# Performance work log

Measured on AMD Instinct MI355X. Metric: run time of the kernel, lower is better.

The kernel has to match this reference:

```python
import jax, jax.numpy as jnp
import numpy as np

NR, NA = 2, 1                 # num_raw, num_angle
QDIM = NR + 2 * NA            # 4: [r, x1=cos(th), x2=sin(th)]
DQ = NR + NA                  # 3: [dr, dth]
D = 2 * NR + 3 * NA           # 7: full state dim
HID = 256
EPS = 1e-6


def setup_inputs() -> dict:
    key = jax.random.key(0)
    ks = jax.random.split(key, 4)
    B = 32768
    x = jax.random.normal(ks[0], (B, D), dtype=jnp.float32)
    W0 = jax.random.normal(ks[1], (HID, D), dtype=jnp.float32) / np.sqrt(D)
    b0 = jnp.zeros((HID,), dtype=jnp.float32)
    W1 = jax.random.normal(ks[2], (HID, HID), dtype=jnp.float32) / np.sqrt(HID)
    b1 = jnp.zeros((HID,), dtype=jnp.float32)
    W2 = jax.random.normal(ks[3], (1, HID), dtype=jnp.float32) / np.sqrt(HID)
    b2 = jnp.zeros((1,), dtype=jnp.float32)
    return {"x": x, "W0": W0, "b0": b0, "W1": W1, "b1": b1, "W2": W2, "b2": b2}


def _lnn_forward(x, W0, b0, W1, b1, W2, b2):
    def L_single(xi):  # scalar Lagrangian of one state (D,)
        h = jnp.tanh(W0 @ xi + b0)
        h = jnp.tanh(W1 @ h + b1)
        return (W2 @ h + b2)[0]

    grad_single = jax.grad(L_single)
    gradL = jax.vmap(grad_single)(x)                       # (B, D)

    # Rows of the Hessian corresponding to d/d(dr,dth): (B, DQ, D).
    # Replaces the torch per-row autograd.grad loop with one batched jacfwd.
    def g(xi):
        return grad_single(xi)[QDIM:]                      # dL/d(dr,dth), (DQ,)
    Hrows = jax.vmap(jax.jacfwd(g))(x)                     # (B, DQ, D)

    x1 = x[:, NR:NR + NA]                                  # cos part (B, NA)
    x2 = x[:, NR + NA:QDIM]                                # sin part (B, NA)

    Jr = Hrows[:, :, :NR]                                  # (B, DQ, NR)
    Jx1 = Hrows[:, :, NR:NR + NA]                          # (B, DQ, NA)
    Jx2 = Hrows[:, :, NR + NA:QDIM]                        # (B, DQ, NA)
    Hdq = Hrows[:, :, QDIM:] + EPS * jnp.eye(DQ, dtype=x.dtype)  # (B, DQ, DQ)

    # chain rule back to angle theta: d/dth = -x2 * d/dx1 + x1 * d/dx2
    Jth = -x2[:, None, :] * Jx1 + x1[:, None, :] * Jx2     # (B, DQ, NA)
    Jrth = jnp.concatenate([Jr, Jth], axis=2)              # (B, DQ, DQ)

    dLdr = gradL[:, :NR]
    dLdx1 = gradL[:, NR:NR + NA]
    dLdx2 = gradL[:, NR + NA:QDIM]
    dLdth = -x2 * dLdx1 + x1 * dLdx2
    dLdrdth = jnp.concatenate([dLdr, dLdth], axis=1)       # (B, DQ)

    dq = x[:, QDIM:]                                       # (B, DQ)
    dq_term = jnp.einsum('bij,bj->bi', Jrth, dq)

    rhs = dLdrdth - dq_term                                # control = 0 (no controlNet)
    ddq = jnp.linalg.solve(Hdq, rhs[..., None])[..., 0]    # (B, DQ)

    dr = dq[:, :NR]
    dth = dq[:, NR:]
    dx1 = -x2 * dth
    dx2 = x1 * dth
    return jnp.concatenate([dr, dx1, dx2, ddq], axis=1)    # (B, D)


def reference(x, W0, b0, W1, b1, W2, b2):
    return _lnn_forward(x, W0, b0, W1, b1, W2, b2)
```

## Files before the change

kernel.cpp:

```cpp
#include <hip/hip_runtime.h>
#include <math.h>

#define HID 256
#define EPS_REG 1e-6

typedef __attribute__((ext_vector_type(8))) short short8;
typedef __attribute__((ext_vector_type(4))) short short4v;
typedef __attribute__((ext_vector_type(4))) float v4f;

#define MFMA_BF16(a, b, c) __builtin_amdgcn_mfma_f32_16x16x32_bf16((a), (b), (c), 0, 0, 0)

__device__ __forceinline__ float fast_tanh(float z) {
    const float e = __expf(2.0f * z);
    const float d = e + 1.0f;
    float r = __builtin_amdgcn_rcpf(d);
    r = r * (2.0f - d * r);
    return fmaf(-2.0f, r, 1.0f);
}

__device__ __forceinline__ float rtn_bf16(float v, short* s) {
    unsigned r = (__float_as_uint(v) + 0x8000u) & 0xFFFF0000u;
    *s = (short)(r >> 16);
    return __uint_as_float(r);
}
__device__ __forceinline__ void split3(float v, short* a, short* b, short* c) {
    float f0 = rtn_bf16(v, a);
    float r1 = v - f0;
    float f1 = rtn_bf16(r1, b);
    float r2 = r1 - f1;
    (void)rtn_bf16(r2, c);
}

__global__ void prep_w1_frags(const float* __restrict__ W1, short* __restrict__ ws) {
    const int gid   = blockIdx.x * 128 + threadIdx.x;
    const int lane  = gid & 63;
    const int ks    = (gid >> 6) & 7;
    const int rt    = (gid >> 9) & 15;
    const int which = gid >> 13;
    const int m = lane & 15, q = lane >> 4;

    float v[8];
    if (which == 0) {
        const float* p = W1 + (size_t)(rt*16 + m)*HID + ks*32 + q*8;
        const float4 va = *(const float4*)(p);
        const float4 vb = *(const float4*)(p + 4);
        v[0]=va.x; v[1]=va.y; v[2]=va.z; v[3]=va.w;
        v[4]=vb.x; v[5]=vb.y; v[6]=vb.z; v[7]=vb.w;
    } else {
        const float* p = W1 + (size_t)(ks*32 + q*8)*HID + rt*16 + m;
#pragma unroll
        for (int t = 0; t < 8; ++t) v[t] = p[(size_t)t*HID];
    }
    short8 h8, m8, l8;
#pragma unroll
    for (int t = 0; t < 8; ++t) {
        short sh, sm, sl;
        split3(v[t], &sh, &sm, &sl);
        h8[t] = sh; m8[t] = sm; l8[t] = sl;
    }
    const size_t base = (size_t)which*3*65536 + ((size_t)(rt*8 + ks)*64 + lane)*8;
    *(short8*)(ws + base)          = h8;
    *(short8*)(ws + base + 65536)  = m8;
    *(short8*)(ws + base + 131072) = l8;
}

#define FRAG_NT_STRIDE 13056
#define FRAG_BUF_STRIDE 4352
#define BFRAG_SHORTS 26112
#define M0H_FLOATS 2304
#define PIPE_LDS_BYTES 122880

__device__ __forceinline__ void lnn_phase0(const float* __restrict__ x,
    const float* __restrict__ W0, const float* __restrict__ b0,
    int samp_base, short* __restrict__ Bf, float* __restrict__ M0, int tid)
{
    const int j  = tid & 255;
    const int s0 = (tid >> 8) * 4;
    float w0r[7];
#pragma unroll
    for (int d = 0; d < 7; ++d) w0r[d] = W0[j*7 + d];
    const float bj = b0[j];
    const int kbase = (j >> 3)*136 + (j & 7);
#pragma unroll
    for (int si = 0; si < 4; ++si) {
        const int s = s0 + si;
        const float* xs = x + (size_t)(samp_base + s)*7;
        float z = bj;
#pragma unroll
        for (int d = 0; d < 7; ++d) z = fmaf(w0r[d], xs[d], z);
        const float h  = fast_tanh(z);
        const float sg = 1.0f - h*h;
        M0[j*9 + s] = h;
        const int nt = s >> 2;
        const int cb = (s & 3) * 4;
        float vals[4] = {h, sg*w0r[4], sg*w0r[5], sg*w0r[6]};
#pragma unroll
        for (int comp = 0; comp < 4; ++comp) {
            short sh, sm, sl;
            split3(vals[comp], &sh, &sm, &sl);
            const int a = nt*FRAG_NT_STRIDE + kbase + (cb + comp)*8;
            Bf[a]                     = sh;
            Bf[a + FRAG_BUF_STRIDE]   = sm;
            Bf[a + 2*FRAG_BUF_STRIDE] = sl;
        }
    }
}

__device__ __forceinline__ void lnn_mm(const short8* __restrict__ Ah,
    const short8* __restrict__ Am, const short8* __restrict__ Al,
    const short* __restrict__ Bf, int w, int lane, int boff, v4f acc[2][2])
{
    short8 pah[2][2], pam[2][2], pal[2][2];
#pragma unroll
    for (int rtl = 0; rtl < 2; ++rtl) {
        const size_t fi = ((size_t)((w*2 + rtl)*8))*64 + lane;
        pah[0][rtl] = Ah[fi]; pam[0][rtl] = Am[fi]; pal[0][rtl] = Al[fi];
    }
#pragma unroll
    for (int ks = 0; ks < 8; ++ks) {
        const int cur = ks & 1, nxt = cur ^ 1;
        if (ks < 7) {
#pragma unroll
            for (int rtl = 0; rtl < 2; ++rtl) {
                const size_t fi = ((size_t)((w*2 + rtl)*8 + ks + 1))*64 + lane;
                pah[nxt][rtl] = Ah[fi]; pam[nxt][rtl] = Am[fi]; pal[nxt][rtl] = Al[fi];
            }
        }
        short8 bh[2], bm[2], bl[2];
#pragma unroll
        for (int nt = 0; nt < 2; ++nt) {
            const int a = nt*FRAG_NT_STRIDE + ks*544 + boff;
            bh[nt] = *(const short8*)(&Bf[a]);
            bm[nt] = *(const short8*)(&Bf[a + FRAG_BUF_STRIDE]);
            bl[nt] = *(const short8*)(&Bf[a + 2*FRAG_BUF_STRIDE]);
        }
#pragma unroll
        for (int rtl = 0; rtl < 2; ++rtl) {
            const short8 ah = pah[cur][rtl];
            const short8 am = pam[cur][rtl];
            const short8 al = pal[cur][rtl];
#pragma unroll
            for (int nt = 0; nt < 2; ++nt) {
                acc[rtl][nt] = MFMA_BF16(ah, bl[nt], acc[rtl][nt]);
                acc[rtl][nt] = MFMA_BF16(al, bh[nt], acc[rtl][nt]);
                acc[rtl][nt] = MFMA_BF16(am, bm[nt], acc[rtl][nt]);
                acc[rtl][nt] = MFMA_BF16(am, bh[nt], acc[rtl][nt]);
                acc[rtl][nt] = MFMA_BF16(ah, bm[nt], acc[rtl][nt]);
                acc[rtl][nt] = MFMA_BF16(ah, bh[nt], acc[rtl][nt]);
            }
        }
    }
}

__device__ __forceinline__ void lnn_epi1(v4f acc[2][2], short* __restrict__ Bf,
    const float* __restrict__ b1, const float* __restrict__ W2,
    int w, int lane, int q, int c)
{
    const int myreg = c & 3;
#pragma unroll
    for (int rtl = 0; rtl < 2; ++rtl) {
        const int base = (w*2 + rtl)*16;
        float b1r[4], w2r[4];
#pragma unroll
        for (int r = 0; r < 4; ++r) {
            b1r[r] = b1[base + q*4 + r];
            w2r[r] = W2[base + q*4 + r];
        }
        const int G  = (base >> 3) + (q >> 1);
        const int tq = (q & 1) * 4;
#pragma unroll
        for (int nt = 0; nt < 2; ++nt) {
            short4v ph, pm, pl;
#pragma unroll
            for (int r = 0; r < 4; ++r) {
                const float z0 = __shfl(acc[rtl][nt][r] + b1r[r], lane & ~3, 64);
                const float h1 = fast_tanh(z0);
                const float s1 = 1.0f - h1*h1;
                const float av = acc[rtl][nt][r];
                const float u  = (myreg == 0) ? (w2r[r]*s1)
                                              : (-2.0f*w2r[r]*h1*s1)*av;
                short sh, sm, sl;
                split3(u, &sh, &sm, &sl);
                ph[r] = sh; pm[r] = sm; pl[r] = sl;
            }
            const int a = nt*FRAG_NT_STRIDE + G*136 + c*8 + tq;
            *(short4v*)(&Bf[a])                     = ph;
            *(short4v*)(&Bf[a + FRAG_BUF_STRIDE])   = pm;
            *(short4v*)(&Bf[a + 2*FRAG_BUF_STRIDE]) = pl;
        }
    }
}

__device__ __forceinline__ void lnn_epi2(v4f acc2[2][2], short* __restrict__ Bf,
    const float* __restrict__ M0, const float* __restrict__ W0,
    int w, int lane, int q, int c)
{
    float* U0 = (float*)Bf;
#pragma unroll
    for (int rtl = 0; rtl < 2; ++rtl) {
#pragma unroll
        for (int reg = 0; reg < 4; ++reg) {
            const int j = (w*2 + rtl)*16 + q*4 + reg;
            const float w0sel = W0[j*7 + 3 + (c & 3)];
#pragma unroll
            for (int nt = 0; nt < 2; ++nt) {
                const int s = nt*4 + (c >> 2);
                const float pv = acc2[rtl][nt][reg];
                const float p0 = __shfl(pv, lane & ~3, 64);
                const float h0 = M0[j*9 + s];
                const float sg = 1.0f - h0*h0;
                const float t2 = -2.0f * p0 * h0 * sg;
                const float res = ((c & 3) == 0) ? (p0*sg)
                                                 : fmaf(pv, sg, t2 * w0sel);
                U0[j*36 + s*4 + (c & 3)] = res;
            }
        }
    }
}

__device__ __forceinline__ void lnn_phase3(const float* __restrict__ x,
    const float* __restrict__ W0, short* __restrict__ Bf,
    int samp_base, float* __restrict__ out, int w, int tid)
{
    const float* U0 = (const float*)Bf;
    float* scratch = ((float*)Bf) + 9216 + w * 425;
    const int t = tid & 63;
    float part[25];
#pragma unroll
    for (int qq = 0; qq < 25; ++qq) part[qq] = 0.0f;

#pragma unroll
    for (int m = 0; m < 4; ++m) {
        const int j = t + 64*m;
        const float4 uv = *(const float4*)(&U0[j*36 + w*4]);
        float w0d[7];
#pragma unroll
        for (int d = 0; d < 7; ++d) w0d[d] = W0[j*7 + d];
#pragma unroll
        for (int d = 0; d < 4; ++d) part[d] = fmaf(uv.x, w0d[d], part[d]);
#pragma unroll
        for (int d = 0; d < 7; ++d) {
            part[4  + d] = fmaf(uv.y, w0d[d], part[4  + d]);
            part[11 + d] = fmaf(uv.z, w0d[d], part[11 + d]);
            part[18 + d] = fmaf(uv.w, w0d[d], part[18 + d]);
        }
    }
#pragma unroll
    for (int off = 1; off <= 2; off <<= 1)
#pragma unroll
        for (int qq = 0; qq < 25; ++qq)
            part[qq] += __shfl_xor(part[qq], off, 64);
    {
        const int quad = t >> 2;
        if ((t & 3) == 0) {
#pragma unroll
            for (int e = 0; e < 25; ++e)
                scratch[e*17 + quad] = part[e];
        }
    }
    if (t < 25) {
        float tot = 0.0f;
#pragma unroll
        for (int k = 0; k < 16; ++k) tot += scratch[t*17 + k];
        scratch[t*17 + 16] = tot;
    }

    if (t == 0) {
        double g[25];
#pragma unroll
        for (int e = 0; e < 25; ++e) g[e] = (double)scratch[e*17 + 16];

        const float* xs = x + (size_t)(samp_base + w)*7;
        const double x1 = xs[2], x2 = xs[3];
        const double dq0 = xs[4], dq1 = xs[5], dth = xs[6];

        double M[3][3], rhs[3];
#pragma unroll
        for (int i = 0; i < 3; ++i) {
            const double J0 = g[4 + i*7 + 0];
            const double J1 = g[4 + i*7 + 1];
            const double J2 = -x2*g[4 + i*7 + 2] + x1*g[4 + i*7 + 3];
            const double dL = (i == 0) ? g[0]
                            : (i == 1) ? g[1]
                            : (-x2*g[2] + x1*g[3]);
            M[i][0] = g[4 + i*7 + 4] + (i == 0 ? EPS_REG : 0.0);
            M[i][1] = g[4 + i*7 + 5] + (i == 1 ? EPS_REG : 0.0);
            M[i][2] = g[4 + i*7 + 6] + (i == 2 ? EPS_REG : 0.0);
            rhs[i]  = dL - (J0*dq0 + J1*dq1 + J2*dth);
        }
        const double c00 = M[1][1]*M[2][2] - M[1][2]*M[2][1];
        const double c01 = M[1][2]*M[2][0] - M[1][0]*M[2][2];
        const double c02 = M[1][0]*M[2][1] - M[1][1]*M[2][0];
        const double det = M[0][0]*c00 + M[0][1]*c01 + M[0][2]*c02;
        const double inv = 1.0 / det;
        const double c10 = M[0][2]*M[2][1] - M[0][1]*M[2][2];
        const double c11 = M[0][0]*M[2][2] - M[0][2]*M[2][0];
        const double c12 = M[0][1]*M[2][0] - M[0][0]*M[2][1];
        const double c20 = M[0][1]*M[1][2] - M[0][2]*M[1][1];
        const double c21 = M[0][2]*M[1][0] - M[0][0]*M[1][2];
        const double c22 = M[0][0]*M[1][1] - M[0][1]*M[1][0];
        const double sol0 = (c00*rhs[0] + c10*rhs[1] + c20*rhs[2]) * inv;
        const double sol1 = (c01*rhs[0] + c11*rhs[1] + c21*rhs[2]) * inv;
        const double sol2 = (c02*rhs[0] + c12*rhs[1] + c22*rhs[2]) * inv;

        float* o = out + (size_t)(samp_base + w)*7;
        o[0] = (float)dq0;
        o[1] = (float)dq1;
        o[2] = (float)(-x2*dth);
        o[3] = (float)( x1*dth);
        o[4] = (float)sol0;
        o[5] = (float)sol1;
        o[6] = (float)sol2;
    }
}

__global__ __launch_bounds__(1024, 4)
void lnn_pipe(const float* __restrict__ x,
              const float* __restrict__ W0, const float* __restrict__ b0,
              const float* __restrict__ b1, const float* __restrict__ W2,
              const short* __restrict__ ws,
              float* __restrict__ out)
{
    extern __shared__ __align__(16) short smem[];

    const int tid  = threadIdx.x;
    const int w16  = tid >> 6;
    const int isA  = (w16 < 8) ? 1 : 0;
    const int w    = w16 & 7;
    const int lane = tid & 63;
    const int gtid = w*64 + lane;

    short* Bf = smem + (isA ? 0 : BFRAG_SHORTS);
    float* M0 = (float*)(smem + 2*BFRAG_SHORTS) + (isA ? 0 : M0H_FLOATS);
    const int samp0 = blockIdx.x * 16 + (isA ? 0 : 8);

    const short8* A1h = (const short8*)ws;
    const short8* A1m = A1h + 8192;
    const short8* A1l = A1h + 16384;
    const short8* A2h = A1h + 24576;
    const short8* A2m = A1h + 32768;
    const short8* A2l = A1h + 40960;

    const int q = lane >> 4;
    const int c = lane & 15;
    const int boff = q*136 + c*8;

    if (isA) lnn_phase0(x, W0, b0, samp0, Bf, M0, gtid);
    __syncthreads();

    v4f acc[2][2];
#pragma unroll
    for (int r = 0; r < 2; ++r)
#pragma unroll
        for (int n = 0; n < 2; ++n) acc[r][n] = (v4f){0.f, 0.f, 0.f, 0.f};
    if (isA) lnn_mm(A1h, A1m, A1l, Bf, w, lane, boff, acc);
    else     lnn_phase0(x, W0, b0, samp0, Bf, M0, gtid);
    __syncthreads();

    if (isA) lnn_epi1(acc, Bf, b1, W2, w, lane, q, c);
    else     lnn_mm(A1h, A1m, A1l, Bf, w, lane, boff, acc);
    __syncthreads();

    v4f acc2[2][2];
#pragma unroll
    for (int r = 0; r < 2; ++r)
#pragma unroll
        for (int n = 0; n < 2; ++n) acc2[r][n] = (v4f){0.f, 0.f, 0.f, 0.f};
    if (isA) lnn_mm(A2h, A2m, A2l, Bf, w, lane, boff, acc2);
    else     lnn_epi1(acc, Bf, b1, W2, w, lane, q, c);
    __syncthreads();

    if (isA) lnn_epi2(acc2, Bf, M0, W0, w, lane, q, c);
    else     lnn_mm(A2h, A2m, A2l, Bf, w, lane, boff, acc2);
    __syncthreads();

    if (isA) lnn_phase3(x, W0, Bf, samp0, out, w, gtid);
    else     lnn_epi2(acc2, Bf, M0, W0, w, lane, q, c);
    __syncthreads();

    if (!isA) lnn_phase3(x, W0, Bf, samp0, out, w, gtid);
}

__global__ __launch_bounds__(512, 4)
void lnn_mfma(const float* __restrict__ x,
              const float* __restrict__ W0, const float* __restrict__ b0,
              const float* __restrict__ b1, const float* __restrict__ W2,
              const short* __restrict__ ws,
              float* __restrict__ out)
{
    __shared__ __align__(16) short Bfrag[26112];
    __shared__ float M0h[HID * 9];

    const int tid   = threadIdx.x;
    const int samp0 = blockIdx.x * 8;
    const int lane  = tid & 63;
    const int w     = tid >> 6;

    lnn_phase0(x, W0, b0, samp0, Bfrag, M0h, tid);
    __syncthreads();

    const short8* A1h = (const short8*)ws;
    const short8* A1m = A1h + 8192;
    const short8* A1l = A1h + 16384;
    const short8* A2h = A1h + 24576;
    const short8* A2m = A1h + 32768;
    const short8* A2l = A1h + 40960;

    const int q = lane >> 4;
    const int c = lane & 15;
    const int boff = q*136 + c*8;

    v4f acc[2][2];
#pragma unroll
    for (int r = 0; r < 2; ++r)
#pragma unroll
        for (int n = 0; n < 2; ++n) acc[r][n] = (v4f){0.f, 0.f, 0.f, 0.f};
    lnn_mm(A1h, A1m, A1l, Bfrag, w, lane, boff, acc);
    __syncthreads();

    lnn_epi1(acc, Bfrag, b1, W2, w, lane, q, c);
    __syncthreads();

    v4f acc2[2][2];
#pragma unroll
    for (int r = 0; r < 2; ++r)
#pragma unroll
        for (int n = 0; n < 2; ++n) acc2[r][n] = (v4f){0.f, 0.f, 0.f, 0.f};
    lnn_mm(A2h, A2m, A2l, Bfrag, w, lane, boff, acc2);
    __syncthreads();

    lnn_epi2(acc2, Bfrag, M0h, W0, w, lane, q, c);
    __syncthreads();

    lnn_phase3(x, W0, Bfrag, samp0, out, w, tid);
}

#define TS8 8
#define SCP 36

__global__ void transpose_w1(const float* __restrict__ W1, float* __restrict__ W1T) {
    __shared__ float tile[32][33];
    const int bx = blockIdx.x & 7;
    const int by = blockIdx.x >> 3;
    const int tx = threadIdx.x & 31;
    const int ty = threadIdx.x >> 5;
#pragma unroll
    for (int q = 0; q < 4; ++q)
        tile[ty + q*8][tx] = W1[(by*32 + ty + q*8)*HID + bx*32 + tx];
    __syncthreads();
#pragma unroll
    for (int q = 0; q < 4; ++q)
        W1T[(bx*32 + ty + q*8)*HID + by*32 + tx] = tile[tx][ty + q*8];
}

__global__ __launch_bounds__(256, 2)
void lnn_fused(const float* __restrict__ x,
               const float* __restrict__ W0, const float* __restrict__ b0,
               const float* __restrict__ W1, const float* __restrict__ b1,
               const float* __restrict__ W2,
               const float* __restrict__ W1T, const int useT,
               float* __restrict__ out)
{
    __shared__ float M0[HID * SCP];
    __shared__ float U [HID * SCP];
    const int tid   = threadIdx.x;
    const int samp0 = blockIdx.x * TS8;
    {
        const int j = tid;
        float w0r[7];
#pragma unroll
        for (int d = 0; d < 7; ++d) w0r[d] = W0[j*7 + d];
        const float bj = b0[j];
#pragma unroll
        for (int s = 0; s < TS8; ++s) {
            const float* xs = x + (size_t)(samp0 + s)*7;
            float z = bj;
#pragma unroll
            for (int d = 0; d < 7; ++d) z = fmaf(w0r[d], xs[d], z);
            const float h  = tanhf(z);
            const float sg = 1.0f - h*h;
            float4 v = {h, sg * w0r[4], sg * w0r[5], sg * w0r[6]};
            *(float4*)(&M0[j*SCP + s*4]) = v;
        }
    }
    __syncthreads();
    const int it = tid & 63;
    const int ct = tid >> 6;
    float acc[4][8];
#pragma unroll
    for (int r = 0; r < 4; ++r)
#pragma unroll
        for (int c = 0; c < 8; ++c) acc[r][c] = 0.0f;
    if (useT) {
#pragma unroll 4
        for (int j = 0; j < HID; ++j) {
            const float4 w4 = *(const float4*)(W1T + (size_t)j*HID + it*4);
            const float4 ma = *(const float4*)(&M0[j*SCP + ct*8]);
            const float4 mb = *(const float4*)(&M0[j*SCP + ct*8 + 4]);
            const float w[4] = {w4.x, w4.y, w4.z, w4.w};
            const float m[8] = {ma.x, ma.y, ma.z, ma.w, mb.x, mb.y, mb.z, mb.w};
#pragma unroll
            for (int r = 0; r < 4; ++r)
#pragma unroll
                for (int c = 0; c < 8; ++c)
                    acc[r][c] = fmaf(w[r], m[c], acc[r][c]);
        }
    } else {
#pragma unroll 2
        for (int j = 0; j < HID; ++j) {
            float w[4];
#pragma unroll
            for (int r = 0; r < 4; ++r) w[r] = W1[(size_t)(it*4 + r)*HID + j];
            const float4 ma = *(const float4*)(&M0[j*SCP + ct*8]);
            const float4 mb = *(const float4*)(&M0[j*SCP + ct*8 + 4]);
            const float m[8] = {ma.x, ma.y, ma.z, ma.w, mb.x, mb.y, mb.z, mb.w};
#pragma unroll
            for (int r = 0; r < 4; ++r)
#pragma unroll
                for (int c = 0; c < 8; ++c)
                    acc[r][c] = fmaf(w[r], m[c], acc[r][c]);
        }
    }
    {
#pragma unroll
        for (int r = 0; r < 4; ++r) {
            const int i = it*4 + r;
            const float b1i = b1[i];
            const float w2i = W2[i];
#pragma unroll
            for (int cs = 0; cs < 2; ++cs) {
                const float z1 = acc[r][cs*4+0] + b1i;
                const float h1 = tanhf(z1);
                const float s1 = 1.0f - h1*h1;
                float4 uv;
                uv.x = w2i * s1;
                const float m2 = -2.0f * w2i * h1 * s1;
                uv.y = m2 * acc[r][cs*4+1];
                uv.z = m2 * acc[r][cs*4+2];
                uv.w = m2 * acc[r][cs*4+3];
                *(float4*)(&U[i*SCP + ct*8 + cs*4]) = uv;
            }
        }
    }
    __syncthreads();
    float acc2[4][8];
#pragma unroll
    for (int r = 0; r < 4; ++r)
#pragma unroll
        for (int c = 0; c < 8; ++c) acc2[r][c] = 0.0f;
#pragma unroll 4
    for (int i = 0; i < HID; ++i) {
        const float4 w4 = *(const float4*)(W1 + (size_t)i*HID + it*4);
        const float4 ua = *(const float4*)(&U[i*SCP + ct*8]);
        const float4 ub = *(const float4*)(&U[i*SCP + ct*8 + 4]);
        const float w[4] = {w4.x, w4.y, w4.z, w4.w};
        const float m[8] = {ua.x, ua.y, ua.z, ua.w, ub.x, ub.y, ub.z, ub.w};
#pragma unroll
        for (int r = 0; r < 4; ++r)
#pragma unroll
            for (int c = 0; c < 8; ++c)
                acc2[r][c] = fmaf(w[r], m[c], acc2[r][c]);
    }
    __syncthreads();
    {
#pragma unroll
        for (int r = 0; r < 4; ++r) {
            const int j = it*4 + r;
#pragma unroll
            for (int cs = 0; cs < 2; ++cs) {
                const int scb = ct*8 + cs*4;
                const float4 mm = *(const float4*)(&M0[j*SCP + scb]);
                const float h0v = mm.x;
                const float sg  = 1.0f - h0v*h0v;
                const float p   = acc2[r][cs*4+0];
                const float t2  = -2.0f * p * h0v;
                float4 uv;
                uv.x = p * sg;
                uv.y = fmaf(acc2[r][cs*4+1], sg, t2 * mm.y);
                uv.z = fmaf(acc2[r][cs*4+2], sg, t2 * mm.z);
                uv.w = fmaf(acc2[r][cs*4+3], sg, t2 * mm.w);
                *(float4*)(&U[j*SCP + scb]) = uv;
            }
        }
    }
    __syncthreads();
    const int s = tid >> 5;
    const int t = tid & 31;
    float part[25];
#pragma unroll
    for (int qq = 0; qq < 25; ++qq) part[qq] = 0.0f;
#pragma unroll
    for (int m = 0; m < 8; ++m) {
        const int j = t + 32*m;
        const float4 uv = *(const float4*)(&U[j*SCP + s*4]);
        float w0d[7];
#pragma unroll
        for (int d = 0; d < 7; ++d) w0d[d] = W0[j*7 + d];
#pragma unroll
        for (int d = 0; d < 4; ++d) part[d] = fmaf(uv.x, w0d[d], part[d]);
#pragma unroll
        for (int d = 0; d < 7; ++d) {
            part[4  + d] = fmaf(uv.y, w0d[d], part[4  + d]);
            part[11 + d] = fmaf(uv.z, w0d[d], part[11 + d]);
            part[18 + d] = fmaf(uv.w, w0d[d], part[18 + d]);
        }
    }
#pragma unroll
    for (int off = 16; off >= 1; off >>= 1)
#pragma unroll
        for (int qq = 0; qq < 25; ++qq)
            part[qq] += __shfl_xor(part[qq], off, 64);
    if (t == 0) {
        const float* xs = x + (size_t)(samp0 + s)*7;
        const double x1 = xs[2], x2 = xs[3];
        const double dq0 = xs[4], dq1 = xs[5], dth = xs[6];
        double A[3][4];
#pragma unroll
        for (int i = 0; i < 3; ++i) {
            const double J0 = part[4 + i*7 + 0];
            const double J1 = part[4 + i*7 + 1];
            const double J2 = -x2*(double)part[4 + i*7 + 2] + x1*(double)part[4 + i*7 + 3];
            const double dL = (i == 0) ? (double)part[0]
                            : (i == 1) ? (double)part[1]
                            : (-x2*(double)part[2] + x1*(double)part[3]);
            A[i][0] = (double)part[4 + i*7 + 4] + (i == 0 ? EPS_REG : 0.0);
            A[i][1] = (double)part[4 + i*7 + 5] + (i == 1 ? EPS_REG : 0.0);
            A[i][2] = (double)part[4 + i*7 + 6] + (i == 2 ? EPS_REG : 0.0);
            A[i][3] = dL - (J0*dq0 + J1*dq1 + J2*dth);
        }
        for (int cc = 0; cc < 2; ++cc) {
            int piv = cc;
            double mx = fabs(A[cc][cc]);
            for (int rr = cc + 1; rr < 3; ++rr) {
                const double v = fabs(A[rr][cc]);
                if (v > mx) { mx = v; piv = rr; }
            }
            if (piv != cc) {
                for (int k2 = 0; k2 < 4; ++k2) {
                    const double tmp = A[cc][k2]; A[cc][k2] = A[piv][k2]; A[piv][k2] = tmp;
                }
            }
            const double inv = 1.0 / A[cc][cc];
            for (int rr = cc + 1; rr < 3; ++rr) {
                const double f = A[rr][cc] * inv;
                for (int k2 = cc + 1; k2 < 4; ++k2) A[rr][k2] -= f * A[cc][k2];
            }
        }
        const double sol2 = A[2][3] / A[2][2];
        const double sol1 = (A[1][3] - A[1][2]*sol2) / A[1][1];
        const double sol0 = (A[0][3] - A[0][1]*sol1 - A[0][2]*sol2) / A[0][0];
        float* o = out + (size_t)(samp0 + s)*7;
        o[0] = (float)dq0;
        o[1] = (float)dq1;
        o[2] = (float)(-x2*dth);
        o[3] = (float)( x1*dth);
        o[4] = (float)sol0;
        o[5] = (float)sol1;
        o[6] = (float)sol2;
    }
}

extern "C" void kernel_launch(void* const* d_in, const int* in_sizes, int n_in,
                              void* d_out, int out_size, void* d_ws, size_t ws_size,
                              hipStream_t stream) {
    const float* x  = (const float*)d_in[0];
    const float* W0 = (const float*)d_in[1];
    const float* b0 = (const float*)d_in[2];
    const float* W1 = (const float*)d_in[3];
    const float* b1 = (const float*)d_in[4];
    const float* W2 = (const float*)d_in[5];
    float* out = (float*)d_out;

    const int B = in_sizes[0] / 7;
    const size_t NEED = 6u * 65536u * sizeof(short);

    static const bool big_lds_ok = [] {
        return hipFuncSetAttribute(reinterpret_cast<const void*>(lnn_pipe),
                                   hipFuncAttributeMaxDynamicSharedMemorySize,
                                   PIPE_LDS_BYTES) == hipSuccess;
    }();

    if (ws_size >= NEED && (B % 16) == 0 && big_lds_ok) {
        short* ws = (short*)d_ws;
        prep_w1_frags<<<128, 128, 0, stream>>>(W1, ws);
        lnn_pipe<<<B / 16, 1024, PIPE_LDS_BYTES, stream>>>(x, W0, b0, b1, W2, ws, out);
    } else if (ws_size >= NEED && (B % 8) == 0) {
        short* ws = (short*)d_ws;
        prep_w1_frags<<<128, 128, 0, stream>>>(W1, ws);
        lnn_mfma<<<B / 8, 512, 0, stream>>>(x, W0, b0, b1, W2, ws, out);
    } else {
        const int useT = (ws_size >= (size_t)HID * HID * sizeof(float)) ? 1 : 0;
        float* W1T = (float*)d_ws;
        if (useT) transpose_w1<<<64, 256, 0, stream>>>(W1, W1T);
        lnn_fused<<<B / TS8, 256, 0, stream>>>(x, W0, b0, W1, b1, W2, W1T, useT, out);
    }
}
```

Measured before the change: 305.6 us.

## Replace lockstep block barriers with per-group LDS barriers and MFMA token handoff

The two 8-wave groups in a 1024-thread block no longer share __syncthreads. Each group now syncs through its own LDS atomic counter barrier, and a token passes between the groups to alternate access to the MFMA matmul phases. This is meant to let each group run its phases at its own pace instead of being held in lockstep by block-wide barriers. The price is spin-wait polling with s_sleep, and tok_wait has a bounded timeout that silently falls through, which could weaken the intended ordering. Launch bounds drop to 1 block per CU.

```diff
diff --git a/kernel.cpp b/kernel.cpp
--- a/kernel.cpp
+++ b/kernel.cpp
@@ -68,7 +68,25 @@
 #define FRAG_BUF_STRIDE 4352
 #define BFRAG_SHORTS 26112
 #define M0H_FLOATS 2304
-#define PIPE_LDS_BYTES 122880
+#define PIPE_LDS_BYTES 122912
+
+__device__ __forceinline__ void gbar(int* ctr, int target) {
+    __threadfence_block();
+    if ((threadIdx.x & 63) == 0)
+        __hip_atomic_fetch_add(ctr, 1, __ATOMIC_ACQ_REL, __HIP_MEMORY_SCOPE_WORKGROUP);
+    while (__hip_atomic_load(ctr, __ATOMIC_ACQUIRE, __HIP_MEMORY_SCOPE_WORKGROUP) < target)
+        __builtin_amdgcn_s_sleep(1);
+}
+__device__ __forceinline__ void tok_wait(int* tok, int g) {
+    for (int i = 0; i < 8192; ++i) {
+        if (__hip_atomic_load(tok, __ATOMIC_ACQUIRE, __HIP_MEMORY_SCOPE_WORKGROUP) == g)
+            return;
+        __builtin_amdgcn_s_sleep(2);
+    }
+}
+__device__ __forceinline__ void tok_set(int* tok, int v) {
+    __hip_atomic_store(tok, v, __ATOMIC_RELEASE, __HIP_MEMORY_SCOPE_WORKGROUP);
+}
 
 __device__ __forceinline__ void lnn_phase0(const float* __restrict__ x,
     const float* __restrict__ W0, const float* __restrict__ b0,
@@ -314,25 +332,35 @@
     }
 }
 
-__global__ __launch_bounds__(1024, 4)
-void lnn_pipe(const float* __restrict__ x,
-              const float* __restrict__ W0, const float* __restrict__ b0,
-              const float* __restrict__ b1, const float* __restrict__ W2,
-              const short* __restrict__ ws,
-              float* __restrict__ out)
+__global__ __launch_bounds__(1024, 1)
+void lnn_pipe2(const float* __restrict__ x,
+               const float* __restrict__ W0, const float* __restrict__ b0,
+               const float* __restrict__ b1, const float* __restrict__ W2,
+               const short* __restrict__ ws,
+               float* __restrict__ out)
 {
     extern __shared__ __align__(16) short smem[];
+    short* BfA = smem;
+    short* BfB = smem + BFRAG_SHORTS;
+    float* M0A = (float*)(smem + 2*BFRAG_SHORTS);
+    float* M0B = M0A + M0H_FLOATS;
+    int*   syn = (int*)(M0B + M0H_FLOATS);
 
     const int tid  = threadIdx.x;
+    if (tid < 3) syn[tid] = 0;
+    __syncthreads();
+
     const int w16  = tid >> 6;
-    const int isA  = (w16 < 8) ? 1 : 0;
+    const int g    = (w16 >= 8) ? 1 : 0;
     const int w    = w16 & 7;
     const int lane = tid & 63;
     const int gtid = w*64 + lane;
 
-    short* Bf = smem + (isA ? 0 : BFRAG_SHORTS);
-    float* M0 = (float*)(smem + 2*BFRAG_SHORTS) + (isA ? 0 : M0H_FLOATS);
-    const int samp0 = blockIdx.x * 16 + (isA ? 0 : 8);
+    short* Bf = g ? BfB : BfA;
+    float* M0 = g ? M0B : M0A;
+    int* arr  = &syn[g];
+    int* tok  = &syn[2];
+    const int samp0 = blockIdx.x * 16 + g*8;
 
     const short8* A1h = (const short8*)ws;
     const short8* A1m = A1h + 8192;
@@ -345,40 +373,35 @@
     const int c = lane & 15;
     const int boff = q*136 + c*8;
 
-    if (isA) lnn_phase0(x, W0, b0, samp0, Bf, M0, gtid);
-    __syncthreads();
+    lnn_phase0(x, W0, b0, samp0, Bf, M0, gtid);
+    gbar(arr, 8*1);
 
     v4f acc[2][2];
 #pragma unroll
     for (int r = 0; r < 2; ++r)
 #pragma unroll
         for (int n = 0; n < 2; ++n) acc[r][n] = (v4f){0.f, 0.f, 0.f, 0.f};
-    if (isA) lnn_mm(A1h, A1m, A1l, Bf, w, lane, boff, acc);
-    else     lnn_phase0(x, W0, b0, samp0, Bf, M0, gtid);
-    __syncthreads();
-
-    if (isA) lnn_epi1(acc, Bf, b1, W2, w, lane, q, c);
-    else     lnn_mm(A1h, A1m, A1l, Bf, w, lane, boff, acc);
-    __syncthreads();
+    tok_wait(tok, g);
+    lnn_mm(A1h, A1m, A1l, Bf, w, lane, boff, acc);
+    gbar(arr, 8*2);
+    if (gtid == 0) tok_set(tok, g ^ 1);
+
+    lnn_epi1(acc, Bf, b1, W2, w, lane, q, c);
+    gbar(arr, 8*3);
 
     v4f acc2[2][2];
 #pragma unroll
     for (int r = 0; r < 2; ++r)
 #pragma unroll
         for (int n = 0; n < 2; ++n) acc2[r][n] = (v4f){0.f, 0.f, 0.f, 0.f};
-    if (isA) lnn_mm(A2h, A2m, A2l, Bf, w, lane, boff, acc2);
-    else     lnn_epi1(acc, Bf, b1, W2, w, lane, q, c);
-    __syncthreads();
-
-    if (isA) lnn_epi2(acc2, Bf, M0, W0, w, lane, q, c);
-    else     lnn_mm(A2h, A2m, A2l, Bf, w, lane, boff, acc2);
-    __syncthreads();
-
-    if (isA) lnn_phase3(x, W0, Bf, samp0, out, w, gtid);
-    else     lnn_epi2(acc2, Bf, M0, W0, w, lane, q, c);
-    __syncthreads();
-
-    if (!isA) lnn_phase3(x, W0, Bf, samp0, out, w, gtid);
+    tok_wait(tok, g);
+    lnn_mm(A2h, A2m, A2l, Bf, w, lane, boff, acc2);
+    gbar(arr, 8*4);
+    if (gtid == 0) tok_set(tok, g ^ 1);
+
+    lnn_epi2(acc2, Bf, M0, W0, w, lane, q, c);
+    gbar(arr, 8*5);
+    lnn_phase3(x, W0, Bf, samp0, out, w, gtid);
 }
 
 __global__ __launch_bounds__(512, 4)
@@ -675,7 +698,7 @@
     const size_t NEED = 6u * 65536u * sizeof(short);
 
     static const bool big_lds_ok = [] {
-        return hipFuncSetAttribute(reinterpret_cast<const void*>(lnn_pipe),
+        return hipFuncSetAttribute(reinterpret_cast<const void*>(lnn_pipe2),
                                    hipFuncAttributeMaxDynamicSharedMemorySize,
                                    PIPE_LDS_BYTES) == hipSuccess;
     }();
@@ -683,7 +706,7 @@
     if (ws_size >= NEED && (B % 16) == 0 && big_lds_ok) {
         short* ws = (short*)d_ws;
         prep_w1_frags<<<128, 128, 0, stream>>>(W1, ws);
-        lnn_pipe<<<B / 16, 1024, PIPE_LDS_BYTES, stream>>>(x, W0, b0, b1, W2, ws, out);
+        lnn_pipe2<<<B / 16, 1024, PIPE_LDS_BYTES, stream>>>(x, W0, b0, b1, W2, ws, out);
     } else if (ws_size >= NEED && (B % 8) == 0) {
         short* ws = (short*)d_ws;
         prep_w1_frags<<<128, 128, 0, stream>>>(W1, ws);
```

Measured after the change: 291.8 us. 1.05x faster.
